# Optimization experiments

Measured on AMD Instinct MI355X. Metric: run time of the kernel, lower is better.

The kernel has to match this reference:

```python
import jax, jax.numpy as jnp
import numpy as np

# ---- hyperparameters (from pars / init_kwargs) ----
ALPHA = 0.9          # synaptic conductance decay (snn.Synaptic alpha)
BETA = 0.8           # membrane decay (snn.Synaptic beta)
BETA_PLUS = 0.9      # pre-synaptic trace decay
BETA_MINUS = 0.9     # post-synaptic trace decay
THRESHOLD = 1.0
W_MIN, W_MAX = 0.0, 1.0
A_PLUS, A_MINUS = 0.008, 0.0008
T, B, IN, N = 350, 128, 784, 400
SPIKE_P = 0.05       # Bernoulli firing probability of the rate-coded input


def setup_inputs() -> dict:
    key = jax.random.key(0)
    k_img, k_w = jax.random.split(key)
    # Poisson/Bernoulli rate-coded MNIST spike train [T, B, IN]
    image = (jax.random.uniform(k_img, (T, B, IN)) < SPIKE_P).astype(jnp.float32)
    # nn.Linear default init U(-1/sqrt(IN), 1/sqrt(IN)) then clamp to [w_min, w_max]
    s = 1.0 / np.sqrt(IN)
    W = jnp.clip(jax.random.uniform(k_w, (N, IN), minval=-s, maxval=s), W_MIN, W_MAX)
    return {"image": image, "W": W}


def reference(image, W):
    """Fused LIF (snntorch Synaptic, reset-by-subtraction) + STDP loop over T steps.

    Returns (W_final, mem_final, syn_final, total_spikes_per_neuron).
    """
    batch = image.shape[1]

    def step(carry, x_t):
        syn, mem, pre_tr, post_tr, W = carry
        # pre-synaptic trace: tr_t = beta_plus * tr_{t-1} + x_t
        pre_tr = BETA_PLUS * pre_tr + x_t                      # [B, IN]
        # linear projection (no bias)
        I_t = jnp.einsum('bi,ni->bn', x_t, W)                  # [B, N]
        # snntorch Synaptic: reset from pre-update mem, subtract mechanism
        reset = (mem > THRESHOLD).astype(mem.dtype)
        syn = ALPHA * syn + I_t
        mem = BETA * mem + syn - reset * THRESHOLD
        spk = (mem > THRESHOLD).astype(mem.dtype)              # [B, N]
        # post-synaptic trace
        post_tr = BETA_MINUS * post_tr + spk
        # STDP: potentiate on post spike x pre trace, depress on pre spike x post trace
        dW = (A_PLUS * jnp.einsum('bn,bi->ni', spk, pre_tr)
              - A_MINUS * jnp.einsum('bn,bi->ni', post_tr, x_t)) / batch
        W = jnp.clip(W + dW, W_MIN, W_MAX)
        return (syn, mem, pre_tr, post_tr, W), spk.sum(axis=0)

    syn0 = jnp.zeros((batch, N), image.dtype)
    mem0 = jnp.zeros((batch, N), image.dtype)
    pre0 = jnp.zeros((batch, IN), image.dtype)
    post0 = jnp.zeros((batch, N), image.dtype)

    (syn, mem, _, _, W_final), spk_counts = jax.lax.scan(
        step, (syn0, mem0, pre0, post0, W), image)
    return W_final, mem, syn, spk_counts.sum(axis=0)
```

## Files before the change

### kernel.cpp

```cpp
#include <hip/hip_runtime.h>
#include <hip/hip_bf16.h>


#define TT    350
#define BB    128
#define INF   784
#define NNEU  400
#define NS    2
#define NTHR  512
#define LCAP  80

#define ALPHA 0.9f
#define BETA  0.8f
#define BPLUS 0.9f
#define BMIN  0.9f
#define CP    (0.008f/128.0f)
#define CM    (0.0008f/128.0f)

__device__ __forceinline__ float bf2f(__hip_bfloat16 v){ return __bfloat162float(v); }

__global__ void k_pretr(const float* __restrict__ img, __hip_bfloat16* __restrict__ pre){
  int idx = blockIdx.x*blockDim.x + threadIdx.x;
  if (idx >= BB*INF) return;
  float v = 0.f;
  for (int t=0;t<TT;t++){
    v = BPLUS*v + img[(size_t)t*(BB*INF) + idx];
    pre[(size_t)t*(BB*INF) + idx] = __float2bfloat16(v);
  }
}

__global__ void k_S(const __hip_bfloat16* __restrict__ pre, float* __restrict__ S){
  int idx = blockIdx.x*blockDim.x + threadIdx.x;
  if (idx >= TT*INF) return;
  int t = idx / INF, i = idx - t*INF;
  const __hip_bfloat16* p = pre + (size_t)t*(BB*INF) + i;
  float s = 0.f;
  for (int b=0;b<BB;b++) s += bf2f(p[(size_t)b*INF]);
  S[idx] = s;
}

__global__ void k_rowlist(const float* __restrict__ img, unsigned short* __restrict__ lists,
                          int* __restrict__ cnts){
  int gid = blockIdx.x*blockDim.x + threadIdx.x;
  int gw = gid >> 6, lane = gid & 63;
  if (gw >= TT*BB) return;
  __shared__ unsigned short buf[4][LCAP];
  int wl = (threadIdx.x >> 6) & 3;
  const float* p = img + (size_t)gw*INF;
  int cnt = 0;
  for (int wdi=0; wdi<13; wdi++){
    int i = wdi*64 + lane;
    bool a = (i < INF) && (p[i] > 0.f);
    unsigned long long bal = __ballot(a);
    int pos = cnt + __popcll(bal & ((1ull<<lane)-1ull));
    if (a && pos < LCAP) buf[wl][pos] = (unsigned short)i;
    cnt += __popcll(bal);
  }
  for (int k = cnt + lane; k < LCAP; k += 64) buf[wl][k] = (unsigned short)INF;
  if (lane == 0) cnts[gw] = (cnt < LCAP) ? cnt : LCAP;
  if (lane < LCAP/2)
    ((unsigned int*)(lists + (size_t)gw*LCAP))[lane] = ((unsigned int*)buf[wl])[lane];
}

__global__ void k_collist(const float* __restrict__ img, unsigned int* __restrict__ collist){
  int idx = blockIdx.x*blockDim.x + threadIdx.x;
  if (idx >= TT*INF) return;
  int t = idx / INF, i = idx - t*INF;
  const float* p = img + (size_t)t*(BB*INF) + i;
  unsigned long long m0=0, m1=0;
  for (int b=0;b<64;b++) m0 |= ((unsigned long long)(p[(size_t)b*INF]      > 0.f)) << b;
  for (int b=0;b<64;b++) m1 |= ((unsigned long long)(p[(size_t)(64+b)*INF] > 0.f)) << b;
  int cnt = __popcll(m0) + __popcll(m1);
  unsigned int w[8];
  w[0] = (unsigned int)cnt; w[1]=0;w[2]=0;w[3]=0;w[4]=0;w[5]=0;w[6]=0;w[7]=0;
  #pragma unroll
  for (int k=1;k<32;k++){
    int bb;
    if (m0){ bb = __builtin_ctzll(m0); m0 &= m0-1; }
    else if (m1){ bb = 64 + __builtin_ctzll(m1); m1 &= m1-1; }
    else bb = 128;
    w[k>>2] |= ((unsigned int)bb) << ((k&3)*8);
  }
  uint4* dst = (uint4*)(collist + (size_t)idx*8);
  uint4 lo; lo.x=w[0]; lo.y=w[1]; lo.z=w[2]; lo.w=w[3];
  uint4 hi; hi.x=w[4]; hi.y=w[5]; hi.z=w[6]; hi.w=w[7];
  dst[0]=lo; dst[1]=hi;
}

__device__ __forceinline__ float potf(unsigned long long ma, unsigned long long mb,
                                      int pc, float Sv,
                                      const __hip_bfloat16* __restrict__ prt, int c){
  bool direct = (pc <= 64);
  unsigned long long m = direct ? ma : ~ma;
  unsigned long long n = direct ? mb : ~mb;
  float acc = 0.f;
  while (m){ int bb = __builtin_ctzll(m); m &= m-1; acc += bf2f(prt[(size_t)bb*INF + c]); }
  while (n){ int bb = __builtin_ctzll(n); n &= n-1; acc += bf2f(prt[(size_t)(64+bb)*INF + c]); }
  return direct ? acc : (Sv - acc);
}

#define G2(W) { float2 a_ = Wp2[(W) & 0xffffu]; I0 += a_.x; I1 += a_.y; \
                float2 b_ = Wp2[(W) >> 16];     I0 += b_.x; I1 += b_.y; }
#define GATHER8(V) { G2((V).x); G2((V).y); G2((V).z); G2((V).w); }

#define DEP4(W) { float2 p_; \
  p_ = postl[(W) & 0xffu];        d0 += p_.x; d1 += p_.y; \
  p_ = postl[((W)>>8) & 0xffu];   d0 += p_.x; d1 += p_.y; \
  p_ = postl[((W)>>16) & 0xffu];  d0 += p_.x; d1 += p_.y; \
  p_ = postl[(W)>>24];            d0 += p_.x; d1 += p_.y; }

#define DOCOL(c, cl, sv) { \
  float d0=0.f, d1=0.f; \
  unsigned int w0_ = (cl).x; \
  { float2 p_; \
    p_ = postl[(w0_>>8) & 0xffu];  d0 += p_.x; d1 += p_.y; \
    p_ = postl[(w0_>>16) & 0xffu]; d0 += p_.x; d1 += p_.y; \
    p_ = postl[w0_>>24];           d0 += p_.x; d1 += p_.y; } \
  DEP4((cl).y); DEP4((cl).z); DEP4((cl).w); \
  int cc_ = (int)(w0_ & 0xffu); \
  if (cc_ > 15){ \
    uint4 e2_ = *(const uint4*)(collist + ((size_t)t*INF + (c))*8 + 4); \
    DEP4(e2_.x); DEP4(e2_.y); DEP4(e2_.z); DEP4(e2_.w); \
  } \
  float pot0_ = potf(s00, s01, pc0, (sv), prt, (c)); \
  float pot1_ = potf(s10, s11, pc1, (sv), prt, (c)); \
  float2 wv_ = Wp2[(c)]; \
  wv_.x = fminf(fmaxf(wv_.x + CP*pot0_ - CM*d0, 0.f), 1.f); \
  wv_.y = fminf(fmaxf(wv_.y + CP*pot1_ - CM*d1, 0.f), 1.f); \
  Wp2[(c)] = wv_; }

__launch_bounds__(NTHR, 1)
__global__ void k_main(const float* __restrict__ Win,
                       const __hip_bfloat16* __restrict__ pre,
                       const float* __restrict__ S,
                       const unsigned short* __restrict__ lists,
                       const int* __restrict__ cnts,
                       const unsigned int* __restrict__ collist,
                       float* __restrict__ out){
  __shared__ float2 Wp2[800];
  __shared__ float2 postl[132];
  __shared__ unsigned long long smQ[2][2];
  __shared__ float cntS[2];

  const int tid  = threadIdx.x;
  const int lane = tid & 63;
  const int wv   = tid >> 6;
  const int q    = lane >> 4;
  const int b    = (wv << 4) | (lane & 15);
  const int n0   = blockIdx.x * NS;

  for (int i = tid; i < 800; i += NTHR){
    float2 w;
    w.x = (i < INF) ? Win[(size_t)n0*INF + i] : 0.f;
    w.y = (i < INF) ? Win[(size_t)(n0+1)*INF + i] : 0.f;
    Wp2[i] = w;
  }
  if (tid < 132){ postl[tid].x = 0.f; postl[tid].y = 0.f; }
  if (tid < 2) cntS[tid] = 0.f;

  const int c0 = tid;
  const int c1 = tid + NTHR;
  const bool has1 = (c1 < INF);

  float syn0=0.f, mem0=0.f, syn1=0.f, mem1=0.f, sc0=0.f, sc1=0.f;

  const unsigned short* lp0 = lists + ((size_t)b)*LCAP + (size_t)q*8;
  uint4 lA = *(const uint4*)lp0;
  uint4 lB = *(const uint4*)(lp0 + 32);
  int cn = cnts[b];
  uint4 cl0 = *(const uint4*)(collist + (size_t)c0*8);
  float sv0 = S[c0];
  uint4 cl1 = cl0; float sv1 = 0.f;
  if (has1){ cl1 = *(const uint4*)(collist + (size_t)c1*8); sv1 = S[c1]; }

  for (int t=0; t<TT; t++){
    __syncthreads();
    float I0 = 0.f, I1 = 0.f;
    GATHER8(lA); GATHER8(lB);
    if (cn > 64 + q*8){
      uint4 lC = *(const uint4*)(lists + ((size_t)t*BB + b)*LCAP + 64 + (size_t)q*8);
      GATHER8(lC);
    }
    int tn = (t+1 < TT) ? t+1 : TT-1;
    const unsigned short* lpn = lists + ((size_t)tn*BB + b)*LCAP + (size_t)q*8;
    uint4 lAn = *(const uint4*)lpn;
    uint4 lBn = *(const uint4*)(lpn + 32);
    int cnn = cnts[tn*BB + b];
    uint4 cl0n = *(const uint4*)(collist + ((size_t)tn*INF + c0)*8);
    float sv0n = S[tn*INF + c0];
    uint4 cl1n = cl0n; float sv1n = 0.f;
    if (has1){ cl1n = *(const uint4*)(collist + ((size_t)tn*INF + c1)*8); sv1n = S[tn*INF + c1]; }

    I0 += __shfl_xor(I0, 16); I0 += __shfl_xor(I0, 32);
    I1 += __shfl_xor(I1, 16); I1 += __shfl_xor(I1, 32);

    float r0 = (mem0 > 1.f) ? 1.f : 0.f;
    syn0 = ALPHA*syn0 + I0;
    mem0 = BETA*mem0 + syn0 - r0;
    float s0 = (mem0 > 1.f) ? 1.f : 0.f;
    float r1 = (mem1 > 1.f) ? 1.f : 0.f;
    syn1 = ALPHA*syn1 + I1;
    mem1 = BETA*mem1 + syn1 - r1;
    float s1 = (mem1 > 1.f) ? 1.f : 0.f;
    unsigned long long bal0 = __ballot(s0 > 0.5f);
    unsigned long long bal1 = __ballot(s1 > 0.5f);
    if (q == 0){
      sc0 += s0; sc1 += s1;
      float2 pv = postl[b];
      pv.x = BMIN*pv.x + s0;
      pv.y = BMIN*pv.y + s1;
      postl[b] = pv;
    }
    if (lane == 0){
      ((unsigned short*)smQ)[wv]     = (unsigned short)(bal0 & 0xffffu);
      ((unsigned short*)smQ)[8 + wv] = (unsigned short)(bal1 & 0xffffu);
    }
    __syncthreads();

    unsigned long long s00 = smQ[0][0], s01 = smQ[0][1];
    unsigned long long s10 = smQ[1][0], s11 = smQ[1][1];
    int pc0 = __popcll(s00) + __popcll(s01);
    int pc1 = __popcll(s10) + __popcll(s11);
    const __hip_bfloat16* prt = pre + (size_t)t*(BB*INF);
    DOCOL(c0, cl0, sv0)
    if (has1) DOCOL(c1, cl1, sv1)

    lA=lAn; lB=lBn; cn=cnn; cl0=cl0n; sv0=sv0n; cl1=cl1n; sv1=sv1n;
  }

  __syncthreads();
  for (int i = tid; i < INF; i += NTHR){
    float2 wvv = Wp2[i];
    out[(size_t)n0*INF + i]       = wvv.x;
    out[(size_t)(n0+1)*INF + i]   = wvv.y;
  }
  if (q == 0){
    out[(size_t)NNEU*INF + (size_t)b*NNEU + n0]                        = mem0;
    out[(size_t)NNEU*INF + (size_t)b*NNEU + n0 + 1]                    = mem1;
    out[(size_t)NNEU*INF + (size_t)BB*NNEU + (size_t)b*NNEU + n0]      = syn0;
    out[(size_t)NNEU*INF + (size_t)BB*NNEU + (size_t)b*NNEU + n0 + 1]  = syn1;
    atomicAdd(&cntS[0], sc0);
    atomicAdd(&cntS[1], sc1);
  }
  __syncthreads();
  if (tid < 2) out[(size_t)NNEU*INF + 2*(size_t)BB*NNEU + n0 + tid] = cntS[tid];
}

extern "C" void kernel_launch(void* const* d_in, const int* in_sizes, int n_in,
                              void* d_out, int out_size, void* d_ws, size_t ws_size,
                              hipStream_t stream) {
  const float* img = (const float*)d_in[0];
  const float* W   = (const float*)d_in[1];
  float* out = (float*)d_out;

  char* ws = (char*)d_ws;
  __hip_bfloat16* pre  = (__hip_bfloat16*)ws;
  float*          S    = (float*)(ws + 70246400);
  unsigned short* lst  = (unsigned short*)(ws + 71344000);
  int*            cnts = (int*)(ws + 78512000);
  unsigned int*   coll = (unsigned int*)(ws + 78691200);

  k_pretr  <<<(BB*INF + 255)/256, 256, 0, stream>>>(img, pre);
  k_S      <<<(TT*INF + 255)/256, 256, 0, stream>>>(pre, S);
  k_rowlist<<<(TT*BB*64)/256,     256, 0, stream>>>(img, lst, cnts);
  k_collist<<<(TT*INF + 255)/256, 256, 0, stream>>>(img, coll);
  k_main   <<<NNEU/NS, NTHR, 0, stream>>>(W, pre, S, lst, cnts, coll, out);
}
```

Baseline: 836.0 us.

## Double block size to 1024 threads, one column and 8 lanes per batch row

Raises the block from 512 to 1024 threads. Each thread now owns a single input column instead of up to two, and each batch row's spike-list gather is split across 8 lanes instead of 4. The intent is to shorten per-thread serial work inside the latency-bound time loop. In exchange, every step adds one shuffle stage, and block-wide syncs now span 16 waves, which could make each barrier costlier. Ballots are now packed into bytes per wave.

```diff
diff --git a/kernel.cpp b/kernel.cpp
--- a/kernel.cpp
+++ b/kernel.cpp
@@ -7,7 +7,7 @@
 #define INF   784
 #define NNEU  400
 #define NS    2
-#define NTHR  512
+#define NTHR  1024
 #define LCAP  80
 
 #define ALPHA 0.9f
@@ -145,54 +145,50 @@
   const int tid  = threadIdx.x;
   const int lane = tid & 63;
   const int wv   = tid >> 6;
-  const int q    = lane >> 4;
-  const int b    = (wv << 4) | (lane & 15);
+  const int q    = lane >> 3;
+  const int b    = (wv << 3) | (lane & 7);
   const int n0   = blockIdx.x * NS;
 
-  for (int i = tid; i < 800; i += NTHR){
+  if (tid < 800){
     float2 w;
-    w.x = (i < INF) ? Win[(size_t)n0*INF + i] : 0.f;
-    w.y = (i < INF) ? Win[(size_t)(n0+1)*INF + i] : 0.f;
-    Wp2[i] = w;
+    w.x = (tid < INF) ? Win[(size_t)n0*INF + tid] : 0.f;
+    w.y = (tid < INF) ? Win[(size_t)(n0+1)*INF + tid] : 0.f;
+    Wp2[tid] = w;
   }
   if (tid < 132){ postl[tid].x = 0.f; postl[tid].y = 0.f; }
   if (tid < 2) cntS[tid] = 0.f;
 
-  const int c0 = tid;
-  const int c1 = tid + NTHR;
-  const bool has1 = (c1 < INF);
+  const int  c0   = tid;
+  const bool hasc = (c0 < INF);
 
   float syn0=0.f, mem0=0.f, syn1=0.f, mem1=0.f, sc0=0.f, sc1=0.f;
 
   const unsigned short* lp0 = lists + ((size_t)b)*LCAP + (size_t)q*8;
   uint4 lA = *(const uint4*)lp0;
-  uint4 lB = *(const uint4*)(lp0 + 32);
   int cn = cnts[b];
-  uint4 cl0 = *(const uint4*)(collist + (size_t)c0*8);
-  float sv0 = S[c0];
-  uint4 cl1 = cl0; float sv1 = 0.f;
-  if (has1){ cl1 = *(const uint4*)(collist + (size_t)c1*8); sv1 = S[c1]; }
+  uint4 cl0; cl0.x=0;cl0.y=0;cl0.z=0;cl0.w=0;
+  float sv0 = 0.f;
+  if (hasc){ cl0 = *(const uint4*)(collist + (size_t)c0*8); sv0 = S[c0]; }
 
   for (int t=0; t<TT; t++){
     __syncthreads();
     float I0 = 0.f, I1 = 0.f;
-    GATHER8(lA); GATHER8(lB);
+    GATHER8(lA);
     if (cn > 64 + q*8){
       uint4 lC = *(const uint4*)(lists + ((size_t)t*BB + b)*LCAP + 64 + (size_t)q*8);
       GATHER8(lC);
     }
     int tn = (t+1 < TT) ? t+1 : TT-1;
-    const unsigned short* lpn = lists + ((size_t)tn*BB + b)*LCAP + (size_t)q*8;
-    uint4 lAn = *(const uint4*)lpn;
-    uint4 lBn = *(const uint4*)(lpn + 32);
+    uint4 lAn = *(const uint4*)(lists + ((size_t)tn*BB + b)*LCAP + (size_t)q*8);
     int cnn = cnts[tn*BB + b];
-    uint4 cl0n = *(const uint4*)(collist + ((size_t)tn*INF + c0)*8);
-    float sv0n = S[tn*INF + c0];
-    uint4 cl1n = cl0n; float sv1n = 0.f;
-    if (has1){ cl1n = *(const uint4*)(collist + ((size_t)tn*INF + c1)*8); sv1n = S[tn*INF + c1]; }
-
-    I0 += __shfl_xor(I0, 16); I0 += __shfl_xor(I0, 32);
-    I1 += __shfl_xor(I1, 16); I1 += __shfl_xor(I1, 32);
+    uint4 cl0n = cl0; float sv0n = sv0;
+    if (hasc){
+      cl0n = *(const uint4*)(collist + ((size_t)tn*INF + c0)*8);
+      sv0n = S[tn*INF + c0];
+    }
+
+    I0 += __shfl_xor(I0, 8); I0 += __shfl_xor(I0, 16); I0 += __shfl_xor(I0, 32);
+    I1 += __shfl_xor(I1, 8); I1 += __shfl_xor(I1, 16); I1 += __shfl_xor(I1, 32);
 
     float r0 = (mem0 > 1.f) ? 1.f : 0.f;
     syn0 = ALPHA*syn0 + I0;
@@ -212,8 +208,8 @@
       postl[b] = pv;
     }
     if (lane == 0){
-      ((unsigned short*)smQ)[wv]     = (unsigned short)(bal0 & 0xffffu);
-      ((unsigned short*)smQ)[8 + wv] = (unsigned short)(bal1 & 0xffffu);
+      ((unsigned char*)smQ)[wv]      = (unsigned char)(bal0 & 0xffu);
+      ((unsigned char*)smQ)[16 + wv] = (unsigned char)(bal1 & 0xffu);
     }
     __syncthreads();
 
@@ -222,17 +218,16 @@
     int pc0 = __popcll(s00) + __popcll(s01);
     int pc1 = __popcll(s10) + __popcll(s11);
     const __hip_bfloat16* prt = pre + (size_t)t*(BB*INF);
-    DOCOL(c0, cl0, sv0)
-    if (has1) DOCOL(c1, cl1, sv1)
-
-    lA=lAn; lB=lBn; cn=cnn; cl0=cl0n; sv0=sv0n; cl1=cl1n; sv1=sv1n;
+    if (hasc) DOCOL(c0, cl0, sv0)
+
+    lA=lAn; cn=cnn; cl0=cl0n; sv0=sv0n;
   }
 
   __syncthreads();
-  for (int i = tid; i < INF; i += NTHR){
-    float2 wvv = Wp2[i];
-    out[(size_t)n0*INF + i]       = wvv.x;
-    out[(size_t)(n0+1)*INF + i]   = wvv.y;
+  if (tid < INF){
+    float2 wvv = Wp2[tid];
+    out[(size_t)n0*INF + tid]       = wvv.x;
+    out[(size_t)(n0+1)*INF + tid]   = wvv.y;
   }
   if (q == 0){
     out[(size_t)NNEU*INF + (size_t)b*NNEU + n0]                        = mem0;
```

New measurement: 718.8 us. -14.0%, faster.
